# Performance work log

Hardware: AMD Instinct MI355X
Metric: run time of the kernel (lower is better)

## Reference

```python
import jax, jax.numpy as jnp
import numpy as np

TEMP = 0.1
EPS = 0.5
N, D, P = 8192, 128, 1


def setup_inputs() -> dict:
    key = jax.random.key(0)
    k1, k2 = jax.random.split(key)
    return {
        "embeddings": jax.random.normal(k1, (N, D), dtype=jnp.float32),
        "properties": jax.random.uniform(k2, (N, P), dtype=jnp.float32),
    }


def reference(embeddings, properties):
    n = embeddings.shape[0]
    # L2-normalize rows, cosine similarity scaled by temperature
    e = embeddings / jnp.linalg.norm(embeddings, axis=1, keepdims=True)
    sim = (e @ e.T) / TEMP  # [N, N]

    # mask from property distances; comparison is non-differentiable in torch,
    # so stop_gradient keeps the jax graph identical (and avoids sqrt(0) nans)
    props = jax.lax.stop_gradient(properties)
    pd2 = jnp.sum((props[:, None, :] - props[None, :, :]) ** 2, axis=-1)  # [N, N]
    # torch.cdist(p=2) gives sqrt(pd2); code then takes .sqrt() again -> pd2**0.25
    prop_dists = jnp.sqrt(jnp.sqrt(pd2)) + 1e-8
    mask = (prop_dists < EPS).astype(sim.dtype)

    eye = jnp.eye(n, dtype=bool)
    mask = jnp.where(eye, 0.0, mask)          # fill_diagonal_(0)
    logits = jnp.where(eye, -1e9, sim)        # fill_diagonal_(-1e9)
    log_probs = jax.nn.log_softmax(logits, axis=1)

    # fused masked per-row mean of -log_probs over positives, then mean over
    # rows that have at least one positive (replaces the python loop)
    counts = mask.sum(axis=1)                      # [N]
    valid = counts > 0
    per_row = -(mask * log_probs).sum(axis=1) / jnp.maximum(counts, 1.0)
    n_valid = valid.sum()
    loss = jnp.where(
        n_valid > 0,
        jnp.sum(jnp.where(valid, per_row, 0.0)) / jnp.maximum(n_valid, 1).astype(per_row.dtype),
        jnp.asarray(0.0, dtype=per_row.dtype),
    )
    return loss
```

## Files before the change

kernel.cpp:

```cpp
#include <hip/hip_runtime.h>
#include <hip/hip_bf16.h>

#define N_ROWS 8192
#define DIM 128

typedef short v8s  __attribute__((ext_vector_type(8)));
typedef float v16f __attribute__((ext_vector_type(16)));
typedef unsigned int u32;

constexpr int NS = 16;
constexpr int CW = N_ROWS / NS;
constexpr int NSLOT = NS;
constexpr int TILE_J = 32;
constexpr int NT = CW / TILE_J;
constexpr int TB = TILE_J * DIM * 2;
constexpr float THRESH = 0.25f;
constexpr float C1 = 14.426950408889634f;

#define GLDS(gptr, lptr, sz)                                                   \
  __builtin_amdgcn_global_load_lds(                                            \
      (const __attribute__((address_space(1))) u32*)(gptr),                    \
      (__attribute__((address_space(3))) u32*)(lptr), sz, 0, 0)

__device__ __forceinline__ unsigned short f2bf(float f) {
  __hip_bfloat16 h = __float2bfloat16(f);
  return __builtin_bit_cast(unsigned short, h);
}

__global__ __launch_bounds__(256) void knorm(const float* __restrict__ emb,
                                             unsigned short* __restrict__ ebf) {
  const int row  = blockIdx.x * 4 + (threadIdx.x >> 6);
  const int lane = threadIdx.x & 63;
  const float2 v = *reinterpret_cast<const float2*>(emb + (size_t)row * DIM + lane * 2);
  float ss = fmaf(v.x, v.x, v.y * v.y);
#pragma unroll
  for (int off = 32; off > 0; off >>= 1) ss += __shfl_xor(ss, off);
  const float rn = 1.0f / sqrtf(ss);
  const unsigned int packed =
      (unsigned int)f2bf(v.x * rn) | ((unsigned int)f2bf(v.y * rn) << 16);
  *reinterpret_cast<unsigned int*>(ebf + (size_t)row * DIM + lane * 2) = packed;
}

__global__ __launch_bounds__(256) void kmain(const unsigned short* __restrict__ ebf,
                                             const float* __restrict__ props,
                                             float* __restrict__ part) {
  const int lane = threadIdx.x & 63;
  const int w    = threadIdx.x >> 6;
  const int l15  = lane & 15;
  const int g4   = lane >> 4;
  const int r31  = lane & 31;
  const int hi   = lane >> 5;
  const int i0   = blockIdx.x * 128;
  const int iw0  = i0 + w * 32;
  const int jbase = blockIdx.y * CW;

  __shared__ __align__(1024) char sA[2 * TB + CW * 4];
  char* sprops = sA + 2 * TB;

  const int icol = iw0 + r31;

  v8s bfr[8];
#pragma unroll
  for (int kk = 0; kk < 8; ++kk)
    bfr[kk] = *reinterpret_cast<const v8s*>(ebf + (size_t)icol * DIM + kk * 16 + hi * 8);
  const float pc = props[icol];

#pragma unroll
  for (int r = 0; r < 2; ++r)
    GLDS(props + jbase + r * 256 + w * 64 + lane, sprops + r * 1024 + w * 256, 4);

  auto stageA = [&](char* base, int tile) {
    const int jrow0 = jbase + tile * TILE_J;
#pragma unroll
    for (int q = 0; q < 2; ++q) {
      const int row  = q * 16 + w * 4 + g4;
      const int colb = (l15 << 4) ^ ((row & 7) << 4);
      GLDS(ebf + (size_t)(jrow0 + row) * DIM + (colb >> 1),
           base + q * 4096 + w * 1024, 16);
    }
  };

  stageA(sA, 0);
  __syncthreads();

  float es2[2] = {0.f, 0.f}, ms2[2] = {0.f, 0.f}, ct2[2] = {0.f, 0.f};
  const int rswz = (r31 & 7) << 4;

  for (int t = 0; t < NT; ++t) {
    if (t + 1 < NT) stageA(sA + ((t + 1) & 1) * TB, t + 1);

    char* base = sA + (t & 1) * TB;
    const int jrow0 = jbase + t * TILE_J;

    v8s af[8];
#pragma unroll
    for (int kk = 0; kk < 8; ++kk)
      af[kk] = *reinterpret_cast<const v8s*>(
          base + r31 * 256 + ((kk * 32 + hi * 16) ^ rswz));

    float pjf[16];
#pragma unroll
    for (int q = 0; q < 4; ++q) {
      const float4 v = *reinterpret_cast<const float4*>(
          sprops + t * 128 + hi * 16 + q * 32);
      pjf[q * 4 + 0] = v.x; pjf[q * 4 + 1] = v.y;
      pjf[q * 4 + 2] = v.z; pjf[q * 4 + 3] = v.w;
    }

    v16f acc = {0.f, 0.f, 0.f, 0.f, 0.f, 0.f, 0.f, 0.f,
                0.f, 0.f, 0.f, 0.f, 0.f, 0.f, 0.f, 0.f};
#pragma unroll
    for (int kk = 0; kk < 8; ++kk)
      acc = __builtin_amdgcn_mfma_f32_32x32x16_bf16(af[kk], bfr[kk], acc, 0, 0, 0);

    if ((unsigned)(jrow0 - i0) < 128u) {
#pragma unroll
      for (int reg = 0; reg < 16; ++reg) {
        const int jr = jrow0 + (reg & 3) + 8 * (reg >> 2) + 4 * hi;
        const float dot = acc[reg];
        const bool  neq = (jr != icol);
        const float ex  = __builtin_amdgcn_exp2f(fmaf(dot, C1, -C1));
        es2[reg & 1] += neq ? ex : 0.f;
        const float mskf = (neq && (fabsf(pc - pjf[reg]) < THRESH)) ? 1.f : 0.f;
        ct2[reg & 1] += mskf;
        ms2[reg & 1] = fmaf(mskf, dot, ms2[reg & 1]);
      }
    } else {
#pragma unroll
      for (int reg = 0; reg < 16; ++reg) {
        const float dot = acc[reg];
        es2[reg & 1] += __builtin_amdgcn_exp2f(fmaf(dot, C1, -C1));
        const float mskf = (fabsf(pc - pjf[reg]) < THRESH) ? 1.f : 0.f;
        ct2[reg & 1] += mskf;
        ms2[reg & 1] = fmaf(mskf, dot, ms2[reg & 1]);
      }
    }
    __syncthreads();
  }

  float es = es2[0] + es2[1];
  float ms = ms2[0] + ms2[1];
  float ct = ct2[0] + ct2[1];
  es += __shfl_xor(es, 32);
  ms += __shfl_xor(ms, 32);
  ct += __shfl_xor(ct, 32);

  if (hi == 0) {
    float* p0 = part + (size_t)blockIdx.y * 3 * N_ROWS;
    p0[icol]              = es;
    p0[N_ROWS + icol]     = ms;
    p0[2 * N_ROWS + icol] = ct;
  }
}

__global__ __launch_bounds__(256) void kreduce(const float* __restrict__ part,
                                               float* __restrict__ bs,
                                               float* __restrict__ bc) {
  const int row = blockIdx.x * 256 + threadIdx.x;
  float es = 0.f, ms = 0.f, ct = 0.f;
#pragma unroll
  for (int sp = 0; sp < NSLOT; ++sp) {
    const float* p0 = part + (size_t)sp * 3 * N_ROWS;
    es += p0[row];
    ms += p0[N_ROWS + row];
    ct += p0[2 * N_ROWS + row];
  }
  const float lse = 10.0f + logf(es);
  const float per = (ct * lse - 10.0f * ms) / fmaxf(ct, 1.0f);
  float val = (ct > 0.f) ? per : 0.f;
  float vld = (ct > 0.f) ? 1.f : 0.f;
#pragma unroll
  for (int off = 32; off > 0; off >>= 1) {
    val += __shfl_xor(val, off);
    vld += __shfl_xor(vld, off);
  }
  __shared__ float sv[4], sc[4];
  const int wid = threadIdx.x >> 6;
  if ((threadIdx.x & 63) == 0) { sv[wid] = val; sc[wid] = vld; }
  __syncthreads();
  if (threadIdx.x == 0) {
    bs[blockIdx.x] = sv[0] + sv[1] + sv[2] + sv[3];
    bc[blockIdx.x] = sc[0] + sc[1] + sc[2] + sc[3];
  }
}

__global__ __launch_bounds__(64) void kfin(const float* __restrict__ bs,
                                           const float* __restrict__ bc,
                                           float* __restrict__ out) {
  const int l = threadIdx.x;
  float s = (l < 32) ? bs[l] : 0.f;
  float c = (l < 32) ? bc[l] : 0.f;
#pragma unroll
  for (int off = 32; off > 0; off >>= 1) {
    s += __shfl_xor(s, off);
    c += __shfl_xor(c, off);
  }
  if (l == 0) out[0] = (c > 0.f) ? (s / c) : 0.f;
}

extern "C" void kernel_launch(void* const* d_in, const int* in_sizes, int n_in,
                              void* d_out, int out_size, void* d_ws, size_t ws_size,
                              hipStream_t stream) {
  const float* emb   = (const float*)d_in[0];
  const float* props = (const float*)d_in[1];
  float* out = (float*)d_out;

  unsigned short* ebf = (unsigned short*)d_ws;
  const size_t EBF_BYTES  = (size_t)N_ROWS * DIM * 2;
  const size_t PART_BYTES = (size_t)NSLOT * 3 * N_ROWS * 4;
  float* part = (float*)((char*)d_ws + EBF_BYTES);
  float* bs   = (float*)((char*)d_ws + EBF_BYTES + PART_BYTES);
  float* bc   = bs + 32;

  knorm<<<N_ROWS / 4, 256, 0, stream>>>(emb, ebf);
  kmain<<<dim3(N_ROWS / 128, NS), 256, 0, stream>>>(ebf, props, part);
  kreduce<<<N_ROWS / 256, 256, 0, stream>>>(part, bs, bc);
  kfin<<<1, 64, 0, stream>>>(bs, bc, out);
}
```

Measured before the change: 46.47 us.

## Widen main-kernel i-tile to 256 rows, stagger j-tile order, pack epilogue math

The main kernel now runs 512 threads (8 waves) per block covering 256 i-rows. Each staged j-tile in LDS is therefore reused by twice as many waves, and the grid has half as many blocks. Each block starts its j-tile loop at a different phase so concurrent blocks read different rows of the bf16 embedding buffer. The epilogue uses packed 2-wide float ops and a squared-distance threshold test in place of fabs, reading props per pair from LDS instead of preloading 16 values. The reduce kernel moves to 64-thread blocks without shared memory, and the final kernel sums 128 partials. Fewer blocks may lower occupancy and load balance across CUs.

Measured after the change: 45.60 us. Within noise of the previous version (-1.9%).

```diff
diff --git a/kernel.cpp b/kernel.cpp
--- a/kernel.cpp
+++ b/kernel.cpp
@@ -6,6 +6,7 @@
 
 typedef short v8s  __attribute__((ext_vector_type(8)));
 typedef float v16f __attribute__((ext_vector_type(16)));
+typedef float v2f  __attribute__((ext_vector_type(2)));
 typedef unsigned int u32;
 
 constexpr int NS = 16;
@@ -14,7 +15,8 @@
 constexpr int TILE_J = 32;
 constexpr int NT = CW / TILE_J;
 constexpr int TB = TILE_J * DIM * 2;
-constexpr float THRESH = 0.25f;
+constexpr int BI = 256;
+constexpr float T2 = 0.0625f;
 constexpr float C1 = 14.426950408889634f;
 
 #define GLDS(gptr, lptr, sz)                                                   \
@@ -41,16 +43,15 @@
   *reinterpret_cast<unsigned int*>(ebf + (size_t)row * DIM + lane * 2) = packed;
 }
 
-__global__ __launch_bounds__(256) void kmain(const unsigned short* __restrict__ ebf,
+__global__ __launch_bounds__(512) void kmain(const unsigned short* __restrict__ ebf,
                                              const float* __restrict__ props,
                                              float* __restrict__ part) {
-  const int lane = threadIdx.x & 63;
-  const int w    = threadIdx.x >> 6;
-  const int l15  = lane & 15;
-  const int g4   = lane >> 4;
+  const int tid  = threadIdx.x;
+  const int lane = tid & 63;
+  const int w    = tid >> 6;
   const int r31  = lane & 31;
   const int hi   = lane >> 5;
-  const int i0   = blockIdx.x * 128;
+  const int i0   = blockIdx.x * BI;
   const int iw0  = i0 + w * 32;
   const int jbase = blockIdx.y * CW;
 
@@ -65,32 +66,29 @@
     bfr[kk] = *reinterpret_cast<const v8s*>(ebf + (size_t)icol * DIM + kk * 16 + hi * 8);
   const float pc = props[icol];
 
-#pragma unroll
-  for (int r = 0; r < 2; ++r)
-    GLDS(props + jbase + r * 256 + w * 64 + lane, sprops + r * 1024 + w * 256, 4);
+  GLDS(props + jbase + tid, sprops + w * 256, 4);
 
   auto stageA = [&](char* base, int tile) {
     const int jrow0 = jbase + tile * TILE_J;
-#pragma unroll
-    for (int q = 0; q < 2; ++q) {
-      const int row  = q * 16 + w * 4 + g4;
-      const int colb = (l15 << 4) ^ ((row & 7) << 4);
-      GLDS(ebf + (size_t)(jrow0 + row) * DIM + (colb >> 1),
-           base + q * 4096 + w * 1024, 16);
-    }
+    const int row   = w * 4 + (lane >> 4);
+    const int colb  = ((lane & 15) << 4) ^ ((row & 7) << 4);
+    GLDS(ebf + (size_t)(jrow0 + row) * DIM + (colb >> 1), base + w * 1024, 16);
   };
 
-  stageA(sA, 0);
+  const int phase = (blockIdx.x * 5) & (NT - 1);
+  stageA(sA, phase);
   __syncthreads();
 
-  float es2[2] = {0.f, 0.f}, ms2[2] = {0.f, 0.f}, ct2[2] = {0.f, 0.f};
+  v2f es2 = {0.f, 0.f}, ms2 = {0.f, 0.f}, ct2 = {0.f, 0.f};
   const int rswz = (r31 & 7) << 4;
+  const v2f c1v = {C1, C1}, mc1v = {-C1, -C1}, pc2 = {pc, pc};
 
   for (int t = 0; t < NT; ++t) {
-    if (t + 1 < NT) stageA(sA + ((t + 1) & 1) * TB, t + 1);
+    const int tt = (t + phase) & (NT - 1);
+    if (t + 1 < NT) stageA(sA + ((t + 1) & 1) * TB, (tt + 1) & (NT - 1));
 
     char* base = sA + (t & 1) * TB;
-    const int jrow0 = jbase + t * TILE_J;
+    const int jrow0 = jbase + tt * TILE_J;
 
     v8s af[8];
 #pragma unroll
@@ -98,49 +96,52 @@
       af[kk] = *reinterpret_cast<const v8s*>(
           base + r31 * 256 + ((kk * 32 + hi * 16) ^ rswz));
 
-    float pjf[16];
-#pragma unroll
-    for (int q = 0; q < 4; ++q) {
-      const float4 v = *reinterpret_cast<const float4*>(
-          sprops + t * 128 + hi * 16 + q * 32);
-      pjf[q * 4 + 0] = v.x; pjf[q * 4 + 1] = v.y;
-      pjf[q * 4 + 2] = v.z; pjf[q * 4 + 3] = v.w;
-    }
-
     v16f acc = {0.f, 0.f, 0.f, 0.f, 0.f, 0.f, 0.f, 0.f,
                 0.f, 0.f, 0.f, 0.f, 0.f, 0.f, 0.f, 0.f};
 #pragma unroll
     for (int kk = 0; kk < 8; ++kk)
       acc = __builtin_amdgcn_mfma_f32_32x32x16_bf16(af[kk], bfr[kk], acc, 0, 0, 0);
 
-    if ((unsigned)(jrow0 - i0) < 128u) {
-#pragma unroll
-      for (int reg = 0; reg < 16; ++reg) {
-        const int jr = jrow0 + (reg & 3) + 8 * (reg >> 2) + 4 * hi;
-        const float dot = acc[reg];
-        const bool  neq = (jr != icol);
-        const float ex  = __builtin_amdgcn_exp2f(fmaf(dot, C1, -C1));
-        es2[reg & 1] += neq ? ex : 0.f;
-        const float mskf = (neq && (fabsf(pc - pjf[reg]) < THRESH)) ? 1.f : 0.f;
-        ct2[reg & 1] += mskf;
-        ms2[reg & 1] = fmaf(mskf, dot, ms2[reg & 1]);
+    if ((unsigned)(jrow0 - i0) < (unsigned)BI) {
+#pragma unroll
+      for (int r = 0; r < 8; ++r) {
+        const int row0 = ((2 * r) & 3) + 8 * (r >> 1) + 4 * hi;
+        const v2f pj2  = *reinterpret_cast<const v2f*>(
+            sprops + ((size_t)tt * 32 + row0) * 4);
+        const v2f dot2 = {acc[2 * r], acc[2 * r + 1]};
+        const v2f arg  = __builtin_elementwise_fma(dot2, c1v, mc1v);
+        const float ex0 = __builtin_amdgcn_exp2f(arg.x);
+        const float ex1 = __builtin_amdgcn_exp2f(arg.y);
+        const int jr0 = jrow0 + row0;
+        const bool neq0 = (jr0 != icol), neq1 = (jr0 + 1 != icol);
+        const v2f exv = {neq0 ? ex0 : 0.f, neq1 ? ex1 : 0.f};
+        es2 += exv;
+        const v2f d = pc2 - pj2, dsq = d * d;
+        const v2f msk = {(neq0 && dsq.x < T2) ? 1.f : 0.f,
+                         (neq1 && dsq.y < T2) ? 1.f : 0.f};
+        ct2 += msk;
+        ms2 = __builtin_elementwise_fma(msk, dot2, ms2);
       }
     } else {
 #pragma unroll
-      for (int reg = 0; reg < 16; ++reg) {
-        const float dot = acc[reg];
-        es2[reg & 1] += __builtin_amdgcn_exp2f(fmaf(dot, C1, -C1));
-        const float mskf = (fabsf(pc - pjf[reg]) < THRESH) ? 1.f : 0.f;
-        ct2[reg & 1] += mskf;
-        ms2[reg & 1] = fmaf(mskf, dot, ms2[reg & 1]);
+      for (int r = 0; r < 8; ++r) {
+        const int row0 = ((2 * r) & 3) + 8 * (r >> 1) + 4 * hi;
+        const v2f pj2  = *reinterpret_cast<const v2f*>(
+            sprops + ((size_t)tt * 32 + row0) * 4);
+        const v2f dot2 = {acc[2 * r], acc[2 * r + 1]};
+        const v2f arg  = __builtin_elementwise_fma(dot2, c1v, mc1v);
+        const v2f exv  = {__builtin_amdgcn_exp2f(arg.x), __builtin_amdgcn_exp2f(arg.y)};
+        es2 += exv;
+        const v2f d = pc2 - pj2, dsq = d * d;
+        const v2f msk = {(dsq.x < T2) ? 1.f : 0.f, (dsq.y < T2) ? 1.f : 0.f};
+        ct2 += msk;
+        ms2 = __builtin_elementwise_fma(msk, dot2, ms2);
       }
     }
     __syncthreads();
   }
 
-  float es = es2[0] + es2[1];
-  float ms = ms2[0] + ms2[1];
-  float ct = ct2[0] + ct2[1];
+  float es = es2.x + es2.y, ms = ms2.x + ms2.y, ct = ct2.x + ct2.y;
   es += __shfl_xor(es, 32);
   ms += __shfl_xor(ms, 32);
   ct += __shfl_xor(ct, 32);
@@ -153,10 +154,10 @@
   }
 }
 
-__global__ __launch_bounds__(256) void kreduce(const float* __restrict__ part,
-                                               float* __restrict__ bs,
-                                               float* __restrict__ bc) {
-  const int row = blockIdx.x * 256 + threadIdx.x;
+__global__ __launch_bounds__(64) void kreduce(const float* __restrict__ part,
+                                              float* __restrict__ bs,
+                                              float* __restrict__ bc) {
+  const int row = blockIdx.x * 64 + threadIdx.x;
   float es = 0.f, ms = 0.f, ct = 0.f;
 #pragma unroll
   for (int sp = 0; sp < NSLOT; ++sp) {
@@ -174,13 +175,9 @@
     val += __shfl_xor(val, off);
     vld += __shfl_xor(vld, off);
   }
-  __shared__ float sv[4], sc[4];
-  const int wid = threadIdx.x >> 6;
-  if ((threadIdx.x & 63) == 0) { sv[wid] = val; sc[wid] = vld; }
-  __syncthreads();
   if (threadIdx.x == 0) {
-    bs[blockIdx.x] = sv[0] + sv[1] + sv[2] + sv[3];
-    bc[blockIdx.x] = sc[0] + sc[1] + sc[2] + sc[3];
+    bs[blockIdx.x] = val;
+    bc[blockIdx.x] = vld;
   }
 }
 
@@ -188,8 +185,8 @@
                                            const float* __restrict__ bc,
                                            float* __restrict__ out) {
   const int l = threadIdx.x;
-  float s = (l < 32) ? bs[l] : 0.f;
-  float c = (l < 32) ? bc[l] : 0.f;
+  float s = bs[l] + bs[l + 64];
+  float c = bc[l] + bc[l + 64];
 #pragma unroll
   for (int off = 32; off > 0; off >>= 1) {
     s += __shfl_xor(s, off);
@@ -210,10 +207,10 @@
   const size_t PART_BYTES = (size_t)NSLOT * 3 * N_ROWS * 4;
   float* part = (float*)((char*)d_ws + EBF_BYTES);
   float* bs   = (float*)((char*)d_ws + EBF_BYTES + PART_BYTES);
-  float* bc   = bs + 32;
+  float* bc   = bs + 128;
 
   knorm<<<N_ROWS / 4, 256, 0, stream>>>(emb, ebf);
-  kmain<<<dim3(N_ROWS / 128, NS), 256, 0, stream>>>(ebf, props, part);
-  kreduce<<<N_ROWS / 256, 256, 0, stream>>>(part, bs, bc);
+  kmain<<<dim3(N_ROWS / BI, NS), 512, 0, stream>>>(ebf, props, part);
+  kreduce<<<N_ROWS / 64, 64, 0, stream>>>(part, bs, bc);
   kfin<<<1, 64, 0, stream>>>(bs, bc, out);
 }
```
